# Kernel tuning notes

Hardware: AMD Instinct MI355X
Metric: run time of the kernel (lower is better)

Reference implementation:

```python
import jax, jax.numpy as jnp
import numpy as np

N = 500_000
E = 5_000_000
DIM = 16
LR = 0.005
THRESHOLD = 0.0


def setup_inputs() -> dict:
    key = jax.random.key(0)
    ks = jax.random.split(key, 8)
    s = 1.0 / np.sqrt(DIM)
    return {
        "x": jax.random.normal(ks[0], (N, DIM), jnp.float32),
        "edge_index": jax.random.randint(ks[1], (2, E), 0, N, dtype=jnp.int32),
        "W1": jax.random.normal(ks[2], (DIM, DIM), jnp.float32) * s,
        "b1": jnp.zeros((DIM,), jnp.float32),
        "W2": jax.random.normal(ks[3], (DIM, DIM), jnp.float32) * s,
        "b2": jnp.zeros((DIM,), jnp.float32),
        "W3": jax.random.normal(ks[4], (DIM, DIM), jnp.float32) * s,
        "b3": jnp.zeros((DIM,), jnp.float32),
        "positive": 0,  # negative sample -> nonzero loss branch
    }


def gcn_conv(x, edge_index, W, b):
    # PyG GCNConv: h = x @ W.T, add self-loops, symmetric norm, aggregate at dst.
    n = x.shape[0]
    loop = jnp.arange(n, dtype=edge_index.dtype)
    src = jnp.concatenate([edge_index[0], loop])
    dst = jnp.concatenate([edge_index[1], loop])
    deg = jax.ops.segment_sum(jnp.ones_like(dst, x.dtype), dst, num_segments=n)
    dinv = jnp.where(deg > 0, jax.lax.rsqrt(deg), 0.0)
    norm = dinv[src] * dinv[dst]  # [E+N]
    h = x @ W.T  # [N, out]
    msg = norm[:, None] * h[src]  # irregular gather, memory-bound
    return jax.ops.segment_sum(msg, dst, num_segments=n) + b


def local_loss(g, positive):
    t = THRESHOLD
    if positive:
        return jnp.where(g > t + 10.0, 0.0,
               jnp.where(g < t - 10.0, t - g, jnp.log1p(jnp.exp(t - g))))
    return jnp.where(g > t + 10.0, t + g,
           jnp.where(g < t - 10.0, 0.0, jnp.log1p(jnp.exp(g + t))))


def reference(x, edge_index, W1, b1, W2, b2, W3, b3, positive):
    # Note: the original computes activation_normalizer(x) and loss_derivative(g)
    # into z/driv_loss but immediately overwrites both -> dead code, omitted.
    agg = jnp.float32(0.0)
    Wc, bc = W1, b1  # conv1 params, updated in-place each layer in the original
    x_cur = x
    for (W, b) in ((W1, b1), (W2, b2), (W3, b3)):
        z = jax.nn.relu(gcn_conv(x_cur, edge_index, W, b))
        goodness = jnp.sum(z * z) / z.shape[1]
        agg = agg + local_loss(goodness, positive)
        d = 2.0 * jnp.abs(z)            # activation_gradient(z)
        wd = d * d                      # weighted_deriv
        dW = x_cur.T @ wd               # [in, out]
        db = jnp.sum(wd, axis=0)
        Wc = Wc - LR * dW.T
        bc = bc - LR * db
        x_cur = z
    return agg, Wc, bc
```

## Files before the change

### kernel.cpp

```cpp
#include <hip/hip_runtime.h>
#include <math.h>

#define TPB 256
#define TPB_P 512
#define LRATE 0.005f

#define LOG_NPB 10
#define NPB (1 << LOG_NPB)
#define CAP 14336
#define CHUNK 4096
#define CPT (CHUNK / TPB_P)

#define LOG_TILE 13
#define NTILE 64

#define FXS  65536.0f
#define FXSI (1.0f / 65536.0f)

#if __has_builtin(__builtin_amdgcn_cvt_f32_fp8) && __has_builtin(__builtin_amdgcn_cvt_pk_fp8_f32)
__device__ __forceinline__ float fp8_dec(unsigned char v) {
    return __builtin_amdgcn_cvt_f32_fp8((int)v, 0);
}
__device__ __forceinline__ unsigned fp8_pk4(float a, float b, float c, float d) {
    int w = __builtin_amdgcn_cvt_pk_fp8_f32(a, b, 0, false);
    w = __builtin_amdgcn_cvt_pk_fp8_f32(c, d, w, true);
    return (unsigned)w;
}
#else
__device__ __forceinline__ unsigned char fp8_enc1(float f) {
    unsigned u = __float_as_uint(f);
    unsigned s = (u >> 24) & 0x80u;
    u &= 0x7FFFFFFFu;
    if (u >= 0x43E00000u) return (unsigned char)(s | 0x7E);
    if (u < 0x3C800000u) {
        float a = __uint_as_float(u);
        int m = (int)rintf(a * 512.f);
        return (unsigned char)(s | (unsigned)m);
    }
    unsigned mant = u & 0x7FFFFFu;
    unsigned rest = mant & 0xFFFFFu;
    unsigned keep = u >> 20;
    keep += (rest > 0x80000u || (rest == 0x80000u && (keep & 1u))) ? 1u : 0u;
    int eb = (int)(keep >> 3) - 127 + 7;
    return (unsigned char)(s | (unsigned)((eb << 3) | (int)(keep & 7u)));
}
__device__ __forceinline__ float fp8_dec(unsigned char v) {
    unsigned s = ((unsigned)(v & 0x80u)) << 24;
    unsigned e = (v >> 3) & 0xFu;
    unsigned m = v & 7u;
    if (e == 0) {
        float r = (float)m * 0.001953125f;
        return (v & 0x80u) ? -r : r;
    }
    return __uint_as_float(s | ((e + 120u) << 23) | (m << 20));
}
__device__ __forceinline__ unsigned fp8_pk4(float a, float b, float c, float d) {
    return (unsigned)fp8_enc1(a) | ((unsigned)fp8_enc1(b) << 8) |
           ((unsigned)fp8_enc1(c) << 16) | ((unsigned)fp8_enc1(d) << 24);
}
#endif

#if __has_builtin(__builtin_amdgcn_cvt_pk_f32_fp8)
typedef float __attribute__((ext_vector_type(2))) f32x2;
__device__ __forceinline__ void fp8_dec4(unsigned w, float& a, float& b, float& c, float& d) {
    f32x2 lo = __builtin_amdgcn_cvt_pk_f32_fp8((int)w, false);
    f32x2 hi = __builtin_amdgcn_cvt_pk_f32_fp8((int)w, true);
    a = lo[0]; b = lo[1]; c = hi[0]; d = hi[1];
}
#else
__device__ __forceinline__ void fp8_dec4(unsigned w, float& a, float& b, float& c, float& d) {
    a = fp8_dec((unsigned char)(w & 0xFFu));
    b = fp8_dec((unsigned char)((w >> 8) & 0xFFu));
    c = fp8_dec((unsigned char)((w >> 16) & 0xFFu));
    d = fp8_dec((unsigned char)((w >> 24) & 0xFFu));
}
#endif

__global__ __launch_bounds__(TPB_P) void k_partition(const int* __restrict__ src,
                                                     const int* __restrict__ dst,
                                                     int* __restrict__ bcur,
                                                     int* __restrict__ grec,
                                                     int E, int nbuck) {
    __shared__ int hist[TPB_P];
    __shared__ int sc[TPB_P];
    __shared__ int lstart[TPB_P];
    __shared__ int lcur[TPB_P];
    __shared__ int gbase[TPB_P];
    __shared__ int lbuf[CHUNK];
    __shared__ unsigned short bbuf[CHUNK];

    int t = threadIdx.x;
    int chunkBase = blockIdx.x * CHUNK;
    hist[t] = 0;
    __syncthreads();

    int myb[CPT], myrec[CPT];
#pragma unroll
    for (int k = 0; k < CPT; k++) {
        int e = chunkBase + k * TPB_P + t;
        if (e < E) {
            int d = dst[e];
            int s = src[e];
            int b = d >> LOG_NPB;
            myb[k] = b;
            myrec[k] = (s << LOG_NPB) | (d & (NPB - 1));
            atomicAdd(&hist[b], 1);
        } else myb[k] = -1;
    }
    __syncthreads();

    int c = hist[t];
    sc[t] = c;
    __syncthreads();
#pragma unroll
    for (int off = 1; off < TPB_P; off <<= 1) {
        int add = (t >= off) ? sc[t - off] : 0;
        __syncthreads();
        sc[t] += add;
        __syncthreads();
    }
    int excl = sc[t] - c;
    lstart[t] = excl;
    lcur[t] = excl;
    if (t < nbuck && c > 0) gbase[t] = atomicAdd(&bcur[t * 16], c);
    __syncthreads();

#pragma unroll
    for (int k = 0; k < CPT; k++) {
        if (myb[k] >= 0) {
            int p = atomicAdd(&lcur[myb[k]], 1);
            lbuf[p] = myrec[k];
            bbuf[p] = (unsigned short)myb[k];
        }
    }
    __syncthreads();

    int total = E - chunkBase; if (total > CHUNK) total = CHUNK;
    for (int p = t; p < total; p += TPB_P) {
        int b = (int)bbuf[p];
        int pos = gbase[b] + (p - lstart[b]);
        if (pos < CAP) grec[(size_t)b * CAP + pos] = lbuf[p];
    }
}

__global__ __launch_bounds__(TPB) void k_sort(const int* __restrict__ bcur,
                                              int* __restrict__ grec) {
    __shared__ int lbuf[CAP];
    __shared__ int obuf[CAP];
    __shared__ int hist[NTILE];
    __shared__ int curp[NTILE];
    int t = threadIdx.x;
    int b = blockIdx.x;
    int cnt = bcur[b * 16]; if (cnt > CAP) cnt = CAP;
    const size_t base = (size_t)b * CAP;

    for (int i = t; i < NTILE; i += TPB) hist[i] = 0;
    __syncthreads();
    for (int i = t; i < cnt; i += TPB) {
        int r = grec[base + i];
        lbuf[i] = r;
        atomicAdd(&hist[((unsigned)r) >> 23], 1);
    }
    __syncthreads();
    if (t == 0) {
        int run = 0;
#pragma unroll
        for (int k = 0; k < NTILE; k++) { int c = hist[k]; curp[k] = run; run += c; }
    }
    __syncthreads();
    for (int i = t; i < cnt; i += TPB) {
        int r = lbuf[i];
        int p = atomicAdd(&curp[((unsigned)r) >> 23], 1);
        obuf[p] = r;
    }
    __syncthreads();
    for (int i = t; i < cnt; i += TPB) grec[base + i] = obuf[i];
}

__global__ __launch_bounds__(TPB) void k_deg(const int* __restrict__ bcur,
                                             const int* __restrict__ grec,
                                             float* __restrict__ dinv, int N) {
    __shared__ int deg[NPB];
    int t = threadIdx.x;
    int b = blockIdx.x;
    int cnt = bcur[b * 16]; if (cnt > CAP) cnt = CAP;
    const size_t recBase = (size_t)b * CAP;
    for (int i = t; i < NPB; i += TPB) deg[i] = 0;
    __syncthreads();
    for (int i = t; i < cnt; i += TPB)
        atomicAdd(&deg[grec[recBase + i] & (NPB - 1)], 1);
    __syncthreads();
    int nodeBase = b << LOG_NPB;
    for (int i = t; i < NPB; i += TPB) {
        int node = nodeBase + i;
        if (node < N) dinv[node] = rsqrtf((float)(deg[i] + 1));
    }
}

__global__ __launch_bounds__(TPB) void k_h(const float* __restrict__ xc,
                                           const float* __restrict__ W,
                                           const float* __restrict__ dinv,
                                           unsigned* __restrict__ hp, int n) {
    __shared__ float sW[256];
    if (threadIdx.x < 256) sW[threadIdx.x] = W[threadIdx.x];
    __syncthreads();
    int i = blockIdx.x * blockDim.x + threadIdx.x;
    int stride = gridDim.x * blockDim.x;
    for (; i < n; i += stride) {
        float x[16];
        const float4* xr = (const float4*)(xc + (size_t)i * 16);
#pragma unroll
        for (int q = 0; q < 4; q++) {
            float4 v = xr[q];
            x[4*q+0] = v.x; x[4*q+1] = v.y; x[4*q+2] = v.z; x[4*q+3] = v.w;
        }
        float di = dinv[i];
        float hv[16];
#pragma unroll
        for (int j = 0; j < 16; j++) {
            float s = 0.f;
#pragma unroll
            for (int k = 0; k < 16; k++) s = fmaf(x[k], sW[j*16 + k], s);
            hv[j] = di * s;
        }
        uint4 w;
        w.x = fp8_pk4(hv[0],  hv[1],  hv[2],  hv[3]);
        w.y = fp8_pk4(hv[4],  hv[5],  hv[6],  hv[7]);
        w.z = fp8_pk4(hv[8],  hv[9],  hv[10], hv[11]);
        w.w = fp8_pk4(hv[12], hv[13], hv[14], hv[15]);
        ((uint4*)hp)[i] = w;
    }
}

__global__ __launch_bounds__(TPB) void k_agg(const int* __restrict__ bcur,
                                             const int* __restrict__ grec,
                                             const float* __restrict__ dinv,
                                             const unsigned* __restrict__ hp32,
                                             const float* __restrict__ b,
                                             const float* __restrict__ xc,
                                             float* __restrict__ z,
                                             float* __restrict__ partial,
                                             int nb, int N) {
    __shared__ int accI[16 * NPB];
    int t = threadIdx.x;
    int bkt = blockIdx.x;
    int cnt = bcur[bkt * 16]; if (cnt > CAP) cnt = CAP;
    const int nodeBase = bkt << LOG_NPB;
    const size_t recBase = (size_t)bkt * CAP;

    {
        int4 zv = make_int4(0, 0, 0, 0);
        int4* a4 = (int4*)accI;
        for (int i = t; i < 16 * NPB / 4; i += TPB) a4[i] = zv;
    }
    __syncthreads();

    int q = t & 3;
    int gi = t >> 2;
    int j0 = q * 4;
    int base = 0;
    for (; base + 512 <= cnt; base += 512) {
        int rec[8];
#pragma unroll
        for (int u = 0; u < 8; u++) rec[u] = grec[recBase + base + u * 64 + gi];
        unsigned w[8];
#pragma unroll
        for (int u = 0; u < 8; u++)
            w[u] = hp32[(size_t)(((unsigned)rec[u]) >> LOG_NPB) * 4 + q];
#pragma unroll
        for (int u = 0; u < 8; u++) {
            int dl = rec[u] & (NPB - 1);
            float f0, f1, f2, f3;
            fp8_dec4(w[u], f0, f1, f2, f3);
            atomicAdd(&accI[(j0 + 0) * NPB + (dl ^ (j0 + 0))], (int)(f0 * FXS));
            atomicAdd(&accI[(j0 + 1) * NPB + (dl ^ (j0 + 1))], (int)(f1 * FXS));
            atomicAdd(&accI[(j0 + 2) * NPB + (dl ^ (j0 + 2))], (int)(f2 * FXS));
            atomicAdd(&accI[(j0 + 3) * NPB + (dl ^ (j0 + 3))], (int)(f3 * FXS));
        }
    }
    for (int e = base + gi; e < cnt; e += 64) {
        int rec = grec[recBase + e];
        unsigned w = hp32[(size_t)(((unsigned)rec) >> LOG_NPB) * 4 + q];
        int dl = rec & (NPB - 1);
        float f0, f1, f2, f3;
        fp8_dec4(w, f0, f1, f2, f3);
        atomicAdd(&accI[(j0 + 0) * NPB + (dl ^ (j0 + 0))], (int)(f0 * FXS));
        atomicAdd(&accI[(j0 + 1) * NPB + (dl ^ (j0 + 1))], (int)(f1 * FXS));
        atomicAdd(&accI[(j0 + 2) * NPB + (dl ^ (j0 + 2))], (int)(f2 * FXS));
        atomicAdd(&accI[(j0 + 3) * NPB + (dl ^ (j0 + 3))], (int)(f3 * FXS));
    }
    __syncthreads();

    const unsigned char* hpB = (const unsigned char*)hp32;
    int j = t & 15;
    int g0 = t >> 4;
    float bj = b[j];
    float accW[16];
#pragma unroll
    for (int k = 0; k < 16; k++) accW[k] = 0.f;
    float accB = 0.f;

    for (int i = g0; i < NPB; i += 16) {
        int node = nodeBase + i;
        if (node >= N) break;
        float sv = fp8_dec(hpB[(size_t)node * 16 + j]);
        float aj = fmaf((float)accI[j * NPB + (i ^ j)], FXSI, sv);
        float zj = fmaxf(fmaf(dinv[node], aj, bj), 0.f);
        z[(size_t)node * 16 + j] = zj;
        float wdj = 4.f * zj * zj;
        accB += wdj;
        const float4* xrow = (const float4*)(xc + (size_t)node * 16);
        float4 x0 = xrow[0], x1 = xrow[1], x2 = xrow[2], x3 = xrow[3];
        accW[0]  = fmaf(x0.x, wdj, accW[0]);  accW[1]  = fmaf(x0.y, wdj, accW[1]);
        accW[2]  = fmaf(x0.z, wdj, accW[2]);  accW[3]  = fmaf(x0.w, wdj, accW[3]);
        accW[4]  = fmaf(x1.x, wdj, accW[4]);  accW[5]  = fmaf(x1.y, wdj, accW[5]);
        accW[6]  = fmaf(x1.z, wdj, accW[6]);  accW[7]  = fmaf(x1.w, wdj, accW[7]);
        accW[8]  = fmaf(x2.x, wdj, accW[8]);  accW[9]  = fmaf(x2.y, wdj, accW[9]);
        accW[10] = fmaf(x2.z, wdj, accW[10]); accW[11] = fmaf(x2.w, wdj, accW[11]);
        accW[12] = fmaf(x3.x, wdj, accW[12]); accW[13] = fmaf(x3.y, wdj, accW[13]);
        accW[14] = fmaf(x3.z, wdj, accW[14]); accW[15] = fmaf(x3.w, wdj, accW[15]);
    }
    __syncthreads();

    float (*red)[17] = (float (*)[17])accI;
#pragma unroll
    for (int k = 0; k < 16; k++) red[t][k] = accW[k];
    red[t][16] = accB;
    __syncthreads();
    int kk = t >> 4;
    int jj = t & 15;
    float s = 0.f;
#pragma unroll
    for (int g = 0; g < 16; g++) s += red[g * 16 + jj][kk];
    partial[(size_t)(kk * 16 + jj) * nb + bkt] = s;
    if (t < 16) {
        float sb = 0.f;
#pragma unroll
        for (int g = 0; g < 16; g++) sb += red[g * 16 + t][16];
        partial[(size_t)(256 + t) * nb + bkt] = sb;
    }
}

__global__ __launch_bounds__(TPB) void k_reduce(const float* __restrict__ partial,
                                                float* __restrict__ acc,
                                                int nb, int total) {
    int wid = (blockIdx.x * blockDim.x + threadIdx.x) >> 6;
    int lane = threadIdx.x & 63;
    if (wid >= total) return;
    const float* p = partial + (size_t)wid * nb;
    float s = 0.f;
    for (int b = lane; b < nb; b += 64) s += p[b];
#pragma unroll
    for (int off = 32; off > 0; off >>= 1) s += __shfl_down(s, off, 64);
    if (lane == 0) acc[wid] = s;
}

__device__ __forceinline__ float local_loss_f(float g, int positive) {
    const float t = 0.0f;
    if (positive) {
        if (g > t + 10.f) return 0.f;
        if (g < t - 10.f) return t - g;
        return log1pf(expf(t - g));
    } else {
        if (g > t + 10.f) return t + g;
        if (g < t - 10.f) return 0.f;
        return log1pf(expf(g + t));
    }
}

__global__ void k_final(const float* __restrict__ W1, const float* __restrict__ b1,
                        const float* __restrict__ acc, const int* __restrict__ positive,
                        float* __restrict__ outv) {
    int t = threadIdx.x;
    if (t < 256) {
        int jj = t >> 4, kk = t & 15;
        float s = 0.f;
#pragma unroll
        for (int l = 0; l < 3; l++) s += acc[l * 272 + kk * 16 + jj];
        outv[1 + t] = W1[t] - LRATE * s;
    }
    if (t < 16) {
        float s = 0.f;
#pragma unroll
        for (int l = 0; l < 3; l++) s += acc[l * 272 + 256 + t];
        outv[257 + t] = b1[t] - LRATE * s;
    }
    if (t == 0) {
        int pos = positive[0];
        float agg = 0.f;
#pragma unroll
        for (int l = 0; l < 3; l++) {
            float g = 0.f;
#pragma unroll
            for (int jj = 0; jj < 16; jj++) g += acc[l * 272 + 256 + jj];
            g *= (1.0f / 64.0f);
            agg += local_loss_f(g, pos);
        }
        outv[0] = agg;
    }
}

extern "C" void kernel_launch(void* const* d_in, const int* in_sizes, int n_in,
                              void* d_out, int out_size, void* d_ws, size_t ws_size,
                              hipStream_t stream) {
    const float* x  = (const float*)d_in[0];
    const int*   ei = (const int*)d_in[1];
    const float* W1 = (const float*)d_in[2];
    const float* b1 = (const float*)d_in[3];
    const float* W2 = (const float*)d_in[4];
    const float* b2 = (const float*)d_in[5];
    const float* W3 = (const float*)d_in[6];
    const float* b3 = (const float*)d_in[7];
    const int* positive = (const int*)d_in[8];
    float* outv = (float*)d_out;

    const int N = in_sizes[0] / 16;
    const int E = in_sizes[1] / 2;
    const int nbuck = (N + NPB - 1) >> LOG_NPB;

    char* ws = (char*)d_ws;
    size_t off = 0;
    auto carve = [&](size_t bytes) -> void* {
        void* p = ws + off;
        off = (off + bytes + 255) & ~(size_t)255;
        return p;
    };
    int*   bcur   = (int*)  carve((size_t)nbuck * 16 * 4);
    int*   grec   = (int*)  carve((size_t)nbuck * CAP * 4);
    float* dinv   = (float*)carve((size_t)N * 4);
    float* acc    = (float*)carve(3 * 272 * 4);
    float* part   = (float*)carve((size_t)3 * 272 * nbuck * 4);
    unsigned* hp  = (unsigned*)carve((size_t)N * 16);
    float* P1     = (float*)carve((size_t)N * 64);
    float* P2     = (float*)carve((size_t)N * 64);

    hipMemsetAsync(bcur, 0, (size_t)nbuck * 16 * 4, stream);

    const int* src = ei;
    const int* dst = ei + E;

    int partBlocks = (E + CHUNK - 1) / CHUNK;
    k_partition<<<partBlocks, TPB_P, 0, stream>>>(src, dst, bcur, grec, E, nbuck);
    k_sort<<<nbuck, TPB, 0, stream>>>(bcur, grec);
    k_deg<<<nbuck, TPB, 0, stream>>>(bcur, grec, dinv, N);

    const float* Ws[3] = {W1, W2, W3};
    const float* bss[3] = {b1, b2, b3};
    float* outs[3] = {P1, P2, P1};

    int nodeBlocks = (N + TPB - 1) / TPB;

    const float* xc = x;
    for (int l = 0; l < 3; l++) {
        k_h<<<nodeBlocks, TPB, 0, stream>>>(xc, Ws[l], dinv, hp, N);
        k_agg<<<nbuck, TPB, 0, stream>>>(bcur, grec, dinv, hp, bss[l],
                                         xc, outs[l],
                                         part + (size_t)l * 272 * nbuck, nbuck, N);
        xc = outs[l];
    }
    int totalElems = 3 * 272;
    k_reduce<<<(totalElems * 64 + TPB - 1) / TPB, TPB, 0, stream>>>(part, acc, nbuck, totalElems);
    k_final<<<1, 256, 0, stream>>>(W1, b1, acc, positive, outv);
}
```

Before: 428.0 us.

## Split aggregation buckets into four sub-blocks and fuse degree count into sort

The sort kernel now bins records by destination sub-range (256 nodes) and source tile, stores the sub-range offsets in spare bcur slots, and computes degree and dinv itself, so the separate k_deg launch is gone. k_agg launches four blocks per bucket, each handling one 256-node sub-range with a 4x smaller LDS accumulator. This is meant to raise occupancy and parallelism, since only about 489 blocks ran before, and to drop one pass over the records. The cost is more partial sums to reduce, a parallel scan with extra barriers in the sort, and lower per-block work.

```diff
diff --git a/kernel.cpp b/kernel.cpp
--- a/kernel.cpp
+++ b/kernel.cpp
@@ -11,7 +11,10 @@
 #define CHUNK 4096
 #define CPT (CHUNK / TPB_P)
 
-#define LOG_TILE 13
+#define LOG_SUB 8
+#define NSUB 256
+#define NBIN 256
+
 #define NTILE 64
 
 #define FXS  65536.0f
@@ -143,53 +146,53 @@
     }
 }
 
-__global__ __launch_bounds__(TPB) void k_sort(const int* __restrict__ bcur,
-                                              int* __restrict__ grec) {
+__global__ __launch_bounds__(TPB) void k_sort(int* __restrict__ bcur,
+                                              int* __restrict__ grec,
+                                              float* __restrict__ dinv, int N) {
     __shared__ int lbuf[CAP];
     __shared__ int obuf[CAP];
-    __shared__ int hist[NTILE];
-    __shared__ int curp[NTILE];
+    __shared__ int deg[NPB];
+    __shared__ int hist[NBIN];
+    __shared__ int curp[NBIN];
+    __shared__ int sc[NBIN];
     int t = threadIdx.x;
     int b = blockIdx.x;
     int cnt = bcur[b * 16]; if (cnt > CAP) cnt = CAP;
     const size_t base = (size_t)b * CAP;
 
-    for (int i = t; i < NTILE; i += TPB) hist[i] = 0;
+    for (int i = t; i < NBIN; i += TPB) hist[i] = 0;
+    for (int i = t; i < NPB; i += TPB) deg[i] = 0;
     __syncthreads();
     for (int i = t; i < cnt; i += TPB) {
         int r = grec[base + i];
         lbuf[i] = r;
-        atomicAdd(&hist[((unsigned)r) >> 23], 1);
-    }
-    __syncthreads();
-    if (t == 0) {
-        int run = 0;
-#pragma unroll
-        for (int k = 0; k < NTILE; k++) { int c = hist[k]; curp[k] = run; run += c; }
-    }
+        int dl = r & (NPB - 1);
+        atomicAdd(&deg[dl], 1);
+        int bin = ((dl >> LOG_SUB) << 6) | (int)(((unsigned)r) >> 23);
+        atomicAdd(&hist[bin], 1);
+    }
+    __syncthreads();
+    if (t < NBIN) sc[t] = hist[t];
+    __syncthreads();
+    for (int off = 1; off < NBIN; off <<= 1) {
+        int v = (t < NBIN && t >= off) ? sc[t - off] : 0;
+        __syncthreads();
+        if (t < NBIN) sc[t] += v;
+        __syncthreads();
+    }
+    if (t < NBIN) curp[t] = sc[t] - hist[t];
+    __syncthreads();
+    if (t < 4) bcur[b * 16 + 8 + t] = curp[t * 64];
     __syncthreads();
     for (int i = t; i < cnt; i += TPB) {
         int r = lbuf[i];
-        int p = atomicAdd(&curp[((unsigned)r) >> 23], 1);
+        int dl = r & (NPB - 1);
+        int bin = ((dl >> LOG_SUB) << 6) | (int)(((unsigned)r) >> 23);
+        int p = atomicAdd(&curp[bin], 1);
         obuf[p] = r;
     }
     __syncthreads();
     for (int i = t; i < cnt; i += TPB) grec[base + i] = obuf[i];
-}
-
-__global__ __launch_bounds__(TPB) void k_deg(const int* __restrict__ bcur,
-                                             const int* __restrict__ grec,
-                                             float* __restrict__ dinv, int N) {
-    __shared__ int deg[NPB];
-    int t = threadIdx.x;
-    int b = blockIdx.x;
-    int cnt = bcur[b * 16]; if (cnt > CAP) cnt = CAP;
-    const size_t recBase = (size_t)b * CAP;
-    for (int i = t; i < NPB; i += TPB) deg[i] = 0;
-    __syncthreads();
-    for (int i = t; i < cnt; i += TPB)
-        atomicAdd(&deg[grec[recBase + i] & (NPB - 1)], 1);
-    __syncthreads();
     int nodeBase = b << LOG_NPB;
     for (int i = t; i < NPB; i += TPB) {
         int node = nodeBase + i;
@@ -241,25 +244,30 @@
                                              float* __restrict__ z,
                                              float* __restrict__ partial,
                                              int nb, int N) {
-    __shared__ int accI[16 * NPB];
+    __shared__ int accI[256 * 17];
     int t = threadIdx.x;
-    int bkt = blockIdx.x;
+    int bkt = blockIdx.x >> 2;
+    int h = blockIdx.x & 3;
     int cnt = bcur[bkt * 16]; if (cnt > CAP) cnt = CAP;
-    const int nodeBase = bkt << LOG_NPB;
+    int rs = bcur[bkt * 16 + 8 + h];
+    int re = (h == 3) ? cnt : bcur[bkt * 16 + 9 + h];
+    if (rs > cnt) rs = cnt;
+    if (re > cnt) re = cnt;
+    const int nodeBase = (bkt << LOG_NPB) + (h << LOG_SUB);
     const size_t recBase = (size_t)bkt * CAP;
 
     {
         int4 zv = make_int4(0, 0, 0, 0);
         int4* a4 = (int4*)accI;
-        for (int i = t; i < 16 * NPB / 4; i += TPB) a4[i] = zv;
+        for (int i = t; i < 16 * NSUB / 4; i += TPB) a4[i] = zv;
     }
     __syncthreads();
 
     int q = t & 3;
     int gi = t >> 2;
     int j0 = q * 4;
-    int base = 0;
-    for (; base + 512 <= cnt; base += 512) {
+    int base = rs;
+    for (; base + 512 <= re; base += 512) {
         int rec[8];
 #pragma unroll
         for (int u = 0; u < 8; u++) rec[u] = grec[recBase + base + u * 64 + gi];
@@ -269,25 +277,25 @@
             w[u] = hp32[(size_t)(((unsigned)rec[u]) >> LOG_NPB) * 4 + q];
 #pragma unroll
         for (int u = 0; u < 8; u++) {
-            int dl = rec[u] & (NPB - 1);
+            int dl = rec[u] & (NSUB - 1);
             float f0, f1, f2, f3;
             fp8_dec4(w[u], f0, f1, f2, f3);
-            atomicAdd(&accI[(j0 + 0) * NPB + (dl ^ (j0 + 0))], (int)(f0 * FXS));
-            atomicAdd(&accI[(j0 + 1) * NPB + (dl ^ (j0 + 1))], (int)(f1 * FXS));
-            atomicAdd(&accI[(j0 + 2) * NPB + (dl ^ (j0 + 2))], (int)(f2 * FXS));
-            atomicAdd(&accI[(j0 + 3) * NPB + (dl ^ (j0 + 3))], (int)(f3 * FXS));
+            atomicAdd(&accI[(j0 + 0) * NSUB + (dl ^ (j0 + 0))], (int)(f0 * FXS));
+            atomicAdd(&accI[(j0 + 1) * NSUB + (dl ^ (j0 + 1))], (int)(f1 * FXS));
+            atomicAdd(&accI[(j0 + 2) * NSUB + (dl ^ (j0 + 2))], (int)(f2 * FXS));
+            atomicAdd(&accI[(j0 + 3) * NSUB + (dl ^ (j0 + 3))], (int)(f3 * FXS));
         }
     }
-    for (int e = base + gi; e < cnt; e += 64) {
+    for (int e = base + gi; e < re; e += 64) {
         int rec = grec[recBase + e];
         unsigned w = hp32[(size_t)(((unsigned)rec) >> LOG_NPB) * 4 + q];
-        int dl = rec & (NPB - 1);
+        int dl = rec & (NSUB - 1);
         float f0, f1, f2, f3;
         fp8_dec4(w, f0, f1, f2, f3);
-        atomicAdd(&accI[(j0 + 0) * NPB + (dl ^ (j0 + 0))], (int)(f0 * FXS));
-        atomicAdd(&accI[(j0 + 1) * NPB + (dl ^ (j0 + 1))], (int)(f1 * FXS));
-        atomicAdd(&accI[(j0 + 2) * NPB + (dl ^ (j0 + 2))], (int)(f2 * FXS));
-        atomicAdd(&accI[(j0 + 3) * NPB + (dl ^ (j0 + 3))], (int)(f3 * FXS));
+        atomicAdd(&accI[(j0 + 0) * NSUB + (dl ^ (j0 + 0))], (int)(f0 * FXS));
+        atomicAdd(&accI[(j0 + 1) * NSUB + (dl ^ (j0 + 1))], (int)(f1 * FXS));
+        atomicAdd(&accI[(j0 + 2) * NSUB + (dl ^ (j0 + 2))], (int)(f2 * FXS));
+        atomicAdd(&accI[(j0 + 3) * NSUB + (dl ^ (j0 + 3))], (int)(f3 * FXS));
     }
     __syncthreads();
 
@@ -300,11 +308,11 @@
     for (int k = 0; k < 16; k++) accW[k] = 0.f;
     float accB = 0.f;
 
-    for (int i = g0; i < NPB; i += 16) {
+    for (int i = g0; i < NSUB; i += 16) {
         int node = nodeBase + i;
         if (node >= N) break;
         float sv = fp8_dec(hpB[(size_t)node * 16 + j]);
-        float aj = fmaf((float)accI[j * NPB + (i ^ j)], FXSI, sv);
+        float aj = fmaf((float)accI[j * NSUB + (i ^ j)], FXSI, sv);
         float zj = fmaxf(fmaf(dinv[node], aj, bj), 0.f);
         z[(size_t)node * 16 + j] = zj;
         float wdj = 4.f * zj * zj;
@@ -332,12 +340,12 @@
     float s = 0.f;
 #pragma unroll
     for (int g = 0; g < 16; g++) s += red[g * 16 + jj][kk];
-    partial[(size_t)(kk * 16 + jj) * nb + bkt] = s;
+    partial[(size_t)(kk * 16 + jj) * nb + blockIdx.x] = s;
     if (t < 16) {
         float sb = 0.f;
 #pragma unroll
         for (int g = 0; g < 16; g++) sb += red[g * 16 + t][16];
-        partial[(size_t)(256 + t) * nb + bkt] = sb;
+        partial[(size_t)(256 + t) * nb + blockIdx.x] = sb;
     }
 }
 
@@ -417,6 +425,7 @@
     const int N = in_sizes[0] / 16;
     const int E = in_sizes[1] / 2;
     const int nbuck = (N + NPB - 1) >> LOG_NPB;
+    const int nagg = nbuck * 4;
 
     char* ws = (char*)d_ws;
     size_t off = 0;
@@ -429,7 +438,7 @@
     int*   grec   = (int*)  carve((size_t)nbuck * CAP * 4);
     float* dinv   = (float*)carve((size_t)N * 4);
     float* acc    = (float*)carve(3 * 272 * 4);
-    float* part   = (float*)carve((size_t)3 * 272 * nbuck * 4);
+    float* part   = (float*)carve((size_t)3 * 272 * nagg * 4);
     unsigned* hp  = (unsigned*)carve((size_t)N * 16);
     float* P1     = (float*)carve((size_t)N * 64);
     float* P2     = (float*)carve((size_t)N * 64);
@@ -441,8 +450,7 @@
 
     int partBlocks = (E + CHUNK - 1) / CHUNK;
     k_partition<<<partBlocks, TPB_P, 0, stream>>>(src, dst, bcur, grec, E, nbuck);
-    k_sort<<<nbuck, TPB, 0, stream>>>(bcur, grec);
-    k_deg<<<nbuck, TPB, 0, stream>>>(bcur, grec, dinv, N);
+    k_sort<<<nbuck, TPB, 0, stream>>>(bcur, grec, dinv, N);
 
     const float* Ws[3] = {W1, W2, W3};
     const float* bss[3] = {b1, b2, b3};
@@ -453,12 +461,12 @@
     const float* xc = x;
     for (int l = 0; l < 3; l++) {
         k_h<<<nodeBlocks, TPB, 0, stream>>>(xc, Ws[l], dinv, hp, N);
-        k_agg<<<nbuck, TPB, 0, stream>>>(bcur, grec, dinv, hp, bss[l],
-                                         xc, outs[l],
-                                         part + (size_t)l * 272 * nbuck, nbuck, N);
+        k_agg<<<nagg, TPB, 0, stream>>>(bcur, grec, dinv, hp, bss[l],
+                                        xc, outs[l],
+                                        part + (size_t)l * 272 * nagg, nagg, N);
         xc = outs[l];
     }
     int totalElems = 3 * 272;
-    k_reduce<<<(totalElems * 64 + TPB - 1) / TPB, TPB, 0, stream>>>(part, acc, nbuck, totalElems);
+    k_reduce<<<(totalElems * 64 + TPB - 1) / TPB, TPB, 0, stream>>>(part, acc, nagg, totalElems);
     k_final<<<1, 256, 0, stream>>>(W1, b1, acc, positive, outv);
 }
```

Result: slower. 452.7 us (+5.8%).
